# Kernel tuning notes

Measured on AMD Instinct MI355X. Metric: run time of the kernel, lower is better.

The kernel has to match this reference:

```python
import jax, jax.numpy as jnp
import numpy as np

N_HEADS = 32
N_KV_HEADS = 8
HEAD_DIM = 64
ROPE_THETA = 500000.0


def _rope_cos_sin(position_ids, head_dim, theta):
    # position_ids: [pb, S] int -> cos/sin [pb, S, head_dim]
    inv_freq = 1.0 / (theta ** (jnp.arange(0, head_dim, 2, dtype=jnp.float32) / head_dim))
    freqs = position_ids.astype(jnp.float32)[:, :, None] * inv_freq[None, None, :]  # [pb,S,D/2]
    emb = jnp.concatenate([freqs, freqs], axis=-1)  # [pb,S,D]
    return jnp.cos(emb), jnp.sin(emb)


def _rotate_half(x):
    d = x.shape[-1] // 2
    return jnp.concatenate([-x[..., d:], x[..., :d]], axis=-1)


def setup_inputs() -> dict:
    key = jax.random.key(0)
    k1, k2, k3, k4, k5 = jax.random.split(key, 5)
    B, S, H = 1, 2048, 2048
    KVD = N_KV_HEADS * HEAD_DIM
    scale = 0.02
    return {
        "hidden_states": jax.random.normal(k1, (B, S, H), jnp.float32),
        "position_ids": jnp.arange(S, dtype=jnp.int64 if jax.config.jax_enable_x64 else jnp.int32)[None, :],
        "Wq": jax.random.normal(k2, (H, H), jnp.float32) * scale,
        "Wk": jax.random.normal(k3, (H, KVD), jnp.float32) * scale,
        "Wv": jax.random.normal(k4, (H, KVD), jnp.float32) * scale,
        "Wo": jax.random.normal(k5, (H, H), jnp.float32) * scale,
    }


def reference(hidden_states, position_ids, Wq, Wk, Wv, Wo):
    B, S, H = hidden_states.shape
    G = N_HEADS // N_KV_HEADS  # GQA group size

    q = (hidden_states @ Wq).reshape(B, S, N_HEADS, HEAD_DIM).transpose(0, 2, 1, 3)      # [B,Hq,S,D]
    k = (hidden_states @ Wk).reshape(B, S, N_KV_HEADS, HEAD_DIM).transpose(0, 2, 1, 3)   # [B,Hk,S,D]
    v = (hidden_states @ Wv).reshape(B, S, N_KV_HEADS, HEAD_DIM).transpose(0, 2, 1, 3)   # [B,Hk,S,D]

    cos, sin = _rope_cos_sin(position_ids, HEAD_DIM, ROPE_THETA)  # [pb,S,D]
    cos = cos[:, None].astype(hidden_states.dtype)  # [pb,1,S,D] broadcasts over heads
    sin = sin[:, None].astype(hidden_states.dtype)
    q = q * cos + _rotate_half(q) * sin
    k = k * cos + _rotate_half(k) * sin

    # GQA without materializing repeated K/V: group query heads by kv head
    qg = q.reshape(B, N_KV_HEADS, G, S, HEAD_DIM)
    scale = 1.0 / jnp.sqrt(jnp.asarray(HEAD_DIM, hidden_states.dtype))
    scores = jnp.einsum('bkgqd,bksd->bkgqs', qg, k) * scale  # [B,Hk,G,S,S]
    causal = jnp.tril(jnp.ones((S, S), bool))
    scores = jnp.where(causal, scores, jnp.asarray(-jnp.inf, scores.dtype))
    probs = jax.nn.softmax(scores, axis=-1)
    out = jnp.einsum('bkgqs,bksd->bkgqd', probs, v)  # [B,Hk,G,S,D]
    out = out.reshape(B, N_HEADS, S, HEAD_DIM).transpose(0, 2, 1, 3).reshape(B, S, H)
    return out @ Wo
```

## Files before the change

kernel.cpp:

```cpp
#include <hip/hip_runtime.h>
#include <hip/hip_bf16.h>
#include <math.h>

#define S_LEN 2048
#define HID   2048
#define NH    32
#define NKV   8
#define HD    64
#define QKD   2560
#define LOG2E 1.44269504f
#define L2THETA_32 0.591611505f

typedef unsigned short u16;
typedef __attribute__((ext_vector_type(8))) short short8;
typedef __attribute__((ext_vector_type(4))) float f32x4;

__device__ __forceinline__ u16 f2bf(float x) {
    union { __hip_bfloat16 b; u16 u; } c; c.b = __float2bfloat16(x); return c.u;
}
__device__ __forceinline__ float bf2f(u16 u) {
    union { unsigned int i; float f; } c; c.i = ((unsigned int)u) << 16; return c.f;
}
__device__ __forceinline__ void async_copy16(void* lds, const void* g) {
    __builtin_amdgcn_global_load_lds((const __attribute__((address_space(1))) unsigned int*)g,
                                     (__attribute__((address_space(3))) unsigned int*)lds,
                                     16, 0, 0);
}

__global__ __launch_bounds__(256)
void cast_bf16(const float* __restrict__ in, u16* __restrict__ out, int n8) {
    int i = blockIdx.x * blockDim.x + threadIdx.x;
    if (i >= n8) return;
    const float4* p = (const float4*)(in + (size_t)i * 8);
    float4 a = p[0], b = p[1];
    short8 o;
    o[0] = f2bf(a.x); o[1] = f2bf(a.y); o[2] = f2bf(a.z); o[3] = f2bf(a.w);
    o[4] = f2bf(b.x); o[5] = f2bf(b.y); o[6] = f2bf(b.z); o[7] = f2bf(b.w);
    *(short8*)(out + (size_t)i * 8) = o;
}

__global__ __launch_bounds__(256)
void transpose_all(const float* __restrict__ Wq, const float* __restrict__ Wk,
                   const float* __restrict__ Wv, const float* __restrict__ Wo,
                   u16* __restrict__ WqkvT, u16* __restrict__ WoT) {
    const float* W; u16* WT; int Nin, xT;
    switch (blockIdx.z) {
        case 0:  W = Wq; WT = WqkvT;                         Nin = 2048; xT = 64; break;
        case 1:  W = Wk; WT = WqkvT + (size_t)2048 * 2048;   Nin = 512;  xT = 16; break;
        case 2:  W = Wv; WT = WqkvT + (size_t)2560 * 2048;   Nin = 512;  xT = 16; break;
        default: W = Wo; WT = WoT;                           Nin = 2048; xT = 64; break;
    }
    if ((int)blockIdx.x >= xT) return;
    __shared__ float tile[32][33];
    const int tx = threadIdx.x & 31, ty = threadIdx.x >> 5;
    const int x = blockIdx.x * 32 + tx;
#pragma unroll
    for (int j = ty; j < 32; j += 8)
        tile[j][tx] = W[(size_t)(blockIdx.y * 32 + j) * Nin + x];
    __syncthreads();
    const int xo = blockIdx.y * 32 + tx;
#pragma unroll
    for (int j = ty; j < 32; j += 8)
        WT[(size_t)(blockIdx.x * 32 + j) * 2048 + xo] = f2bf(tile[tx][j]);
}

__global__ __launch_bounds__(256)
void rope_qk(u16* __restrict__ QK, const int* __restrict__ pos) {
    int idx = blockIdx.x * blockDim.x + threadIdx.x;
    int d = idx & 31;
    int hh = (idx >> 5) % 40;
    int s = idx / (32 * 40);
    if (s >= S_LEN) return;
    float p = (float)pos[s];
    float inv_freq = exp2f(-(float)d * L2THETA_32);
    float ang = p * inv_freq;
    float c = cosf(ang), sn = sinf(ang);
    float sc = (hh < 32) ? 0.125f * LOG2E : 1.0f;
    u16* b = QK + (size_t)s * QKD + hh * HD;
    float x0 = bf2f(b[d]), x1 = bf2f(b[d + 32]);
    b[d]      = f2bf((x0 * c - x1 * sn) * sc);
    b[d + 32] = f2bf((x1 * c + x0 * sn) * sc);
}

template<int MODE>
__global__ __launch_bounds__(256)
void gemm_bt(const u16* __restrict__ A, const u16* __restrict__ Bt,
             void* __restrict__ Cv, u16* __restrict__ Vt, int M, int N, int K) {
    __shared__ __attribute__((aligned(16))) u16 As[2][8192];
    __shared__ __attribute__((aligned(16))) u16 Bs[2][4096];
    const int t = threadIdx.x;
    const int lane = t & 63;
    const int w = t >> 6;
    const int lm = lane & 15, quad = lane >> 4;
    const int row0 = blockIdx.y * 128, col0 = blockIdx.x * 64;
    const int wr = w * 32;

    f32x4 acc[2][4];
#pragma unroll
    for (int i = 0; i < 2; ++i)
#pragma unroll
        for (int j = 0; j < 4; ++j) acc[i][j] = (f32x4){0.f, 0.f, 0.f, 0.f};

    const size_t strideB = (size_t)K * 2;
    const char* Ab = (const char*)(A + (size_t)row0 * K);
    const char* Bb = (const char*)(Bt + (size_t)col0 * K);

    const int srow = t >> 3;
    const int scswz = ((t & 7) ^ (srow & 7)) * 16;

    auto stage = [&](int ks, int buf) {
        const int k0b = ks * 128;
        char* ad = (char*)As[buf] + t * 16;
        char* bd = (char*)Bs[buf] + t * 16;
#pragma unroll
        for (int i = 0; i < 4; ++i)
            async_copy16(ad + i * 4096, Ab + (size_t)(i * 32 + srow) * strideB + k0b + scswz);
#pragma unroll
        for (int i = 0; i < 2; ++i)
            async_copy16(bd + i * 4096, Bb + (size_t)(i * 32 + srow) * strideB + k0b + scswz);
    };

    const int nk = K >> 6;
    stage(0, 0);
    if (nk > 1) stage(1, 1);

    const int fswz = (quad ^ (lm & 7)) << 4;

    for (int kk = 0; kk < nk; ++kk) {
        const int cur = kk & 1;
        if (kk + 1 < nk) { asm volatile("s_waitcnt vmcnt(6)\ns_barrier" ::: "memory"); }
        else             { asm volatile("s_waitcnt vmcnt(0)\ns_barrier" ::: "memory"); }

        short8 af[2][2], bfv[4][2];
#pragma unroll
        for (int i = 0; i < 2; ++i) {
            const char* ar = (const char*)As[cur] + (wr + 16 * i + lm) * 128;
            af[i][0] = *(const short8*)(ar + fswz);
            af[i][1] = *(const short8*)(ar + (fswz ^ 64));
        }
#pragma unroll
        for (int j = 0; j < 4; ++j) {
            const char* br = (const char*)Bs[cur] + (16 * j + lm) * 128;
            bfv[j][0] = *(const short8*)(br + fswz);
            bfv[j][1] = *(const short8*)(br + (fswz ^ 64));
        }
#pragma unroll
        for (int i = 0; i < 2; ++i)
#pragma unroll
            for (int j = 0; j < 4; ++j) {
                acc[i][j] = __builtin_amdgcn_mfma_f32_16x16x32_bf16(af[i][0], bfv[j][0], acc[i][j], 0, 0, 0);
                acc[i][j] = __builtin_amdgcn_mfma_f32_16x16x32_bf16(af[i][1], bfv[j][1], acc[i][j], 0, 0, 0);
            }

        asm volatile("s_waitcnt lgkmcnt(0)\ns_barrier" ::: "memory");
        if (kk + 2 < nk) stage(kk + 2, cur);
    }

    const int cr = quad * 4;
#pragma unroll
    for (int i = 0; i < 2; ++i) {
        const int gr = row0 + wr + 16 * i + cr;
#pragma unroll
        for (int j = 0; j < 4; ++j) {
            const int gc = col0 + 16 * j + lm;
            if (MODE == 0) {
#pragma unroll
                for (int rr = 0; rr < 4; ++rr)
                    ((float*)Cv)[(size_t)(gr + rr) * N + gc] = acc[i][j][rr];
            } else if (gc < 2560) {
#pragma unroll
                for (int rr = 0; rr < 4; ++rr)
                    ((u16*)Cv)[(size_t)(gr + rr) * QKD + gc] = f2bf(acc[i][j][rr]);
            } else {
                const int d = gc - 2560;
                ushort4 vv;
                vv.x = f2bf(acc[i][j][0]); vv.y = f2bf(acc[i][j][1]);
                vv.z = f2bf(acc[i][j][2]); vv.w = f2bf(acc[i][j][3]);
                *(ushort4*)(Vt + (size_t)d * S_LEN + gr) = vv;
            }
        }
    }
}

__global__ __launch_bounds__(256)
void attn_mfma(const u16* __restrict__ QK, const u16* __restrict__ Vtg,
               u16* __restrict__ Ctx) {
    __shared__ __attribute__((aligned(16))) u16 QPs[4096];
    __shared__ __attribute__((aligned(16))) u16 Ks[2][4096];
    __shared__ __attribute__((aligned(16))) u16 Vts[2][4096];

    const int t = threadIdx.x;
    const int lane = t & 63;
    const int w = t >> 6;
    const int lm = lane & 15, quad = lane >> 4;
    const int qt = (gridDim.x - 1) - blockIdx.x;
    const int h = blockIdx.y;
    const int kh = h >> 2;
    const int q0 = qt * 64;
    const int njt = qt + 1;

    const char* Kb = (const char*)(QK + 2048 + kh * HD);
    const char* Vb = (const char*)(Vtg + (size_t)(kh * 64) * S_LEN);

    const int srow = t >> 3;
    const int scswz = ((t & 7) ^ (srow & 7)) * 16;

    {
        const char* qb = (const char*)(QK + h * HD);
        const int qrow = w * 16 + (lane >> 3);
        const int qcs = ((lane & 7) ^ (lane >> 3)) * 16;
#pragma unroll
        for (int k2 = 0; k2 < 2; ++k2)
            async_copy16((char*)QPs + w * 2048 + k2 * 1024 + lane * 16,
                         qb + (size_t)(q0 + qrow + k2 * 8) * (QKD * 2) + qcs);
    }

    auto stage_kv = [&](int jt_, int buf) {
        const int j0_ = jt_ * 64;
        char* kdst = (char*)Ks + buf * 8192 + t * 16;
        char* vdst = (char*)Vts + buf * 8192 + t * 16;
        async_copy16(kdst,        Kb + (size_t)(j0_ + srow)      * (QKD * 2) + scswz);
        async_copy16(kdst + 4096, Kb + (size_t)(j0_ + 32 + srow) * (QKD * 2) + scswz);
        async_copy16(vdst,        Vb + (size_t)srow        * (S_LEN * 2) + j0_ * 2 + scswz);
        async_copy16(vdst + 4096, Vb + (size_t)(32 + srow) * (S_LEN * 2) + j0_ * 2 + scswz);
    };

    stage_kv(0, 0);
    if (njt > 1) {
        stage_kv(1, 1);
        asm volatile("s_waitcnt vmcnt(8)" ::: "memory");
    } else {
        asm volatile("s_waitcnt vmcnt(4)" ::: "memory");
    }

    const int ra = w * 16 + lm;
    const int fswz = ((quad ^ (lm & 7)) << 4);
    const short8 qa0 = *(const short8*)((const char*)QPs + ra * 128 + fswz);
    const short8 qa1 = *(const short8*)((const char*)QPs + ra * 128 + (fswz ^ 64));
    asm volatile("s_waitcnt lgkmcnt(0)" ::: "memory");

    short8 onesf;
    {
        const short ob = (lm == 0) ? (short)0x3F80 : (short)0;
#pragma unroll
        for (int j = 0; j < 8; ++j) onesf[j] = ob;
    }

    f32x4 oa[4], la;
#pragma unroll
    for (int dt = 0; dt < 4; ++dt) oa[dt] = (f32x4){0.f, 0.f, 0.f, 0.f};
    la = (f32x4){0.f, 0.f, 0.f, 0.f};

    for (int jt = 0; jt < njt; ++jt) {
        const int cur = jt & 1;
        if (jt + 1 < njt) { asm volatile("s_waitcnt vmcnt(4)\ns_barrier" ::: "memory"); }
        else              { asm volatile("s_waitcnt vmcnt(0)\ns_barrier" ::: "memory"); }

        const char* Kc = (const char*)Ks + cur * 8192;
        const char* Vc = (const char*)Vts + cur * 8192;

        f32x4 sa[4];
#pragma unroll
        for (int ct = 0; ct < 4; ++ct)
            sa[ct] = (f32x4){-16.f, -16.f, -16.f, -16.f};
#pragma unroll
        for (int ct = 0; ct < 4; ++ct) {
            const char* kr = Kc + (ct * 16 + lm) * 128;
            short8 kf0 = *(const short8*)(kr + fswz);
            short8 kf1 = *(const short8*)(kr + (fswz ^ 64));
            sa[ct] = __builtin_amdgcn_mfma_f32_16x16x32_bf16(kf0, qa0, sa[ct], 0, 0, 0);
            sa[ct] = __builtin_amdgcn_mfma_f32_16x16x32_bf16(kf1, qa1, sa[ct], 0, 0, 0);
        }
        if (jt == qt) {
#pragma unroll
            for (int ct = 0; ct < 4; ++ct) {
                const int kvl = ct * 16 + quad * 4;
#pragma unroll
                for (int r = 0; r < 4; ++r)
                    if (kvl + r > ra) sa[ct][r] = -1e30f;
            }
        }
#pragma unroll
        for (int ct = 0; ct < 4; ++ct) {
            ushort4 pka;
            pka.x = f2bf(__builtin_amdgcn_exp2f(sa[ct][0]));
            pka.y = f2bf(__builtin_amdgcn_exp2f(sa[ct][1]));
            pka.z = f2bf(__builtin_amdgcn_exp2f(sa[ct][2]));
            pka.w = f2bf(__builtin_amdgcn_exp2f(sa[ct][3]));
            const int pc = (((2 * ct + (quad >> 1)) ^ (lm & 7)) << 4) + ((quad & 1) << 3);
            *(ushort4*)((char*)QPs + ra * 128 + pc) = pka;
        }
        const short8 pa0 = *(const short8*)((const char*)QPs + ra * 128 + fswz);
        const short8 pa1 = *(const short8*)((const char*)QPs + ra * 128 + (fswz ^ 64));
#pragma unroll
        for (int dt = 0; dt < 4; ++dt) {
            const char* vr = Vc + (dt * 16 + lm) * 128;
            short8 vf0 = *(const short8*)(vr + fswz);
            short8 vf1 = *(const short8*)(vr + (fswz ^ 64));
            oa[dt] = __builtin_amdgcn_mfma_f32_16x16x32_bf16(vf0, pa0, oa[dt], 0, 0, 0);
            oa[dt] = __builtin_amdgcn_mfma_f32_16x16x32_bf16(vf1, pa1, oa[dt], 0, 0, 0);
        }
        la = __builtin_amdgcn_mfma_f32_16x16x32_bf16(onesf, pa0, la, 0, 0, 0);
        la = __builtin_amdgcn_mfma_f32_16x16x32_bf16(onesf, pa1, la, 0, 0, 0);

        asm volatile("s_waitcnt lgkmcnt(0)\ns_barrier" ::: "memory");
        if (jt + 2 < njt) stage_kv(jt + 2, cur);
    }

    const float inva = 1.f / __shfl(la[0], lm);
    const int rowa = q0 + ra;
#pragma unroll
    for (int dt = 0; dt < 4; ++dt) {
        ushort4 o;
        o.x = f2bf(oa[dt][0] * inva); o.y = f2bf(oa[dt][1] * inva);
        o.z = f2bf(oa[dt][2] * inva); o.w = f2bf(oa[dt][3] * inva);
        *(ushort4*)(Ctx + (size_t)rowa * HID + h * HD + dt * 16 + quad * 4) = o;
    }
}

extern "C" void kernel_launch(void* const* d_in, const int* in_sizes, int n_in,
                              void* d_out, int out_size, void* d_ws, size_t ws_size,
                              hipStream_t stream) {
    const float* X   = (const float*)d_in[0];
    const int*   pos = (const int*)d_in[1];
    const float* Wq  = (const float*)d_in[2];
    const float* Wk  = (const float*)d_in[3];
    const float* Wv  = (const float*)d_in[4];
    const float* Wo  = (const float*)d_in[5];
    float* out = (float*)d_out;

    u16* Xb    = (u16*)d_ws;
    u16* WqkvT = Xb + (size_t)4194304;
    u16* WoT   = WqkvT + (size_t)6291456;
    u16* QK    = WoT + (size_t)4194304;
    u16* Vt    = QK + (size_t)S_LEN * QKD;
    u16* Ctxb  = Xb;

    cast_bf16<<<2048, 256, 0, stream>>>(X, Xb, 524288);
    transpose_all<<<dim3(64, 64, 4), 256, 0, stream>>>(Wq, Wk, Wv, Wo, WqkvT, WoT);

    gemm_bt<1><<<dim3(48, 16), 256, 0, stream>>>(Xb, WqkvT, QK, Vt, 2048, 3072, 2048);

    rope_qk<<<10240, 256, 0, stream>>>(QK, pos);

    attn_mfma<<<dim3(32, 32), 256, 0, stream>>>(QK, Vt, Ctxb);

    gemm_bt<0><<<dim3(32, 16), 256, 0, stream>>>(Ctxb, WoT, out, nullptr, 2048, 2048, 2048);
}
```

Baseline: 230.2 us.

## Fuse RoPE into QKV GEMM epilogue and merge cast with weight transpose

Applies the rotary embedding and the softmax scale directly in the QKV GEMM epilogue, using the fact that each 64-column block holds one whole head. This removes the separate rope kernel and its read-modify-write pass over QK. The activation cast is also folded into the weight-transpose launch as an extra z-slice, saving one launch. The cost is more transcendental math in the GEMM epilogue, and the result is now rounded to bf16 once instead of twice.

```diff
diff --git a/kernel.cpp b/kernel.cpp
--- a/kernel.cpp
+++ b/kernel.cpp
@@ -28,21 +28,21 @@
 }
 
 __global__ __launch_bounds__(256)
-void cast_bf16(const float* __restrict__ in, u16* __restrict__ out, int n8) {
-    int i = blockIdx.x * blockDim.x + threadIdx.x;
-    if (i >= n8) return;
-    const float4* p = (const float4*)(in + (size_t)i * 8);
-    float4 a = p[0], b = p[1];
-    short8 o;
-    o[0] = f2bf(a.x); o[1] = f2bf(a.y); o[2] = f2bf(a.z); o[3] = f2bf(a.w);
-    o[4] = f2bf(b.x); o[5] = f2bf(b.y); o[6] = f2bf(b.z); o[7] = f2bf(b.w);
-    *(short8*)(out + (size_t)i * 8) = o;
-}
-
-__global__ __launch_bounds__(256)
-void transpose_all(const float* __restrict__ Wq, const float* __restrict__ Wk,
-                   const float* __restrict__ Wv, const float* __restrict__ Wo,
-                   u16* __restrict__ WqkvT, u16* __restrict__ WoT) {
+void prep(const float* __restrict__ X, u16* __restrict__ Xb,
+          const float* __restrict__ Wq, const float* __restrict__ Wk,
+          const float* __restrict__ Wv, const float* __restrict__ Wo,
+          u16* __restrict__ WqkvT, u16* __restrict__ WoT) {
+    if (blockIdx.z == 4) {
+        const int i = (blockIdx.y * 64 + (int)blockIdx.x) * 256 + threadIdx.x;
+        if (i >= 524288) return;
+        const float4* p = (const float4*)(X + (size_t)i * 8);
+        float4 a = p[0], b = p[1];
+        short8 o;
+        o[0] = f2bf(a.x); o[1] = f2bf(a.y); o[2] = f2bf(a.z); o[3] = f2bf(a.w);
+        o[4] = f2bf(b.x); o[5] = f2bf(b.y); o[6] = f2bf(b.z); o[7] = f2bf(b.w);
+        *(short8*)(Xb + (size_t)i * 8) = o;
+        return;
+    }
     const float* W; u16* WT; int Nin, xT;
     switch (blockIdx.z) {
         case 0:  W = Wq; WT = WqkvT;                         Nin = 2048; xT = 64; break;
@@ -64,28 +64,11 @@
         WT[(size_t)(blockIdx.x * 32 + j) * 2048 + xo] = f2bf(tile[tx][j]);
 }
 
-__global__ __launch_bounds__(256)
-void rope_qk(u16* __restrict__ QK, const int* __restrict__ pos) {
-    int idx = blockIdx.x * blockDim.x + threadIdx.x;
-    int d = idx & 31;
-    int hh = (idx >> 5) % 40;
-    int s = idx / (32 * 40);
-    if (s >= S_LEN) return;
-    float p = (float)pos[s];
-    float inv_freq = exp2f(-(float)d * L2THETA_32);
-    float ang = p * inv_freq;
-    float c = cosf(ang), sn = sinf(ang);
-    float sc = (hh < 32) ? 0.125f * LOG2E : 1.0f;
-    u16* b = QK + (size_t)s * QKD + hh * HD;
-    float x0 = bf2f(b[d]), x1 = bf2f(b[d + 32]);
-    b[d]      = f2bf((x0 * c - x1 * sn) * sc);
-    b[d + 32] = f2bf((x1 * c + x0 * sn) * sc);
-}
-
 template<int MODE>
 __global__ __launch_bounds__(256)
 void gemm_bt(const u16* __restrict__ A, const u16* __restrict__ Bt,
-             void* __restrict__ Cv, u16* __restrict__ Vt, int M, int N, int K) {
+             void* __restrict__ Cv, u16* __restrict__ Vt,
+             const int* __restrict__ pos, int M, int N, int K) {
     __shared__ __attribute__((aligned(16))) u16 As[2][8192];
     __shared__ __attribute__((aligned(16))) u16 Bs[2][4096];
     const int t = threadIdx.x;
@@ -157,26 +140,51 @@
     }
 
     const int cr = quad * 4;
-#pragma unroll
-    for (int i = 0; i < 2; ++i) {
-        const int gr = row0 + wr + 16 * i + cr;
-#pragma unroll
-        for (int j = 0; j < 4; ++j) {
-            const int gc = col0 + 16 * j + lm;
-            if (MODE == 0) {
+    if (MODE == 0) {
+#pragma unroll
+        for (int i = 0; i < 2; ++i) {
+            const int gr = row0 + wr + 16 * i + cr;
+#pragma unroll
+            for (int j = 0; j < 4; ++j) {
+                const int gc = col0 + 16 * j + lm;
 #pragma unroll
                 for (int rr = 0; rr < 4; ++rr)
                     ((float*)Cv)[(size_t)(gr + rr) * N + gc] = acc[i][j][rr];
-            } else if (gc < 2560) {
-#pragma unroll
-                for (int rr = 0; rr < 4; ++rr)
-                    ((u16*)Cv)[(size_t)(gr + rr) * QKD + gc] = f2bf(acc[i][j][rr]);
-            } else {
-                const int d = gc - 2560;
+            }
+        }
+    } else if (col0 >= 2560) {
+#pragma unroll
+        for (int i = 0; i < 2; ++i) {
+            const int gr = row0 + wr + 16 * i + cr;
+#pragma unroll
+            for (int j = 0; j < 4; ++j) {
+                const int d = col0 + 16 * j + lm - 2560;
                 ushort4 vv;
                 vv.x = f2bf(acc[i][j][0]); vv.y = f2bf(acc[i][j][1]);
                 vv.z = f2bf(acc[i][j][2]); vv.w = f2bf(acc[i][j][3]);
                 *(ushort4*)(Vt + (size_t)d * S_LEN + gr) = vv;
+            }
+        }
+    } else {
+        const float qsc = (col0 < 2048) ? 0.125f * LOG2E : 1.0f;
+        const float invf0 = exp2f(-(float)lm * L2THETA_32);
+        const float invf1 = exp2f(-(float)(16 + lm) * L2THETA_32);
+#pragma unroll
+        for (int i = 0; i < 2; ++i) {
+            const int gr = row0 + wr + 16 * i + cr;
+#pragma unroll
+            for (int rr = 0; rr < 4; ++rr) {
+                const float p = (float)pos[gr + rr];
+                const float a0 = p * invf0, a1 = p * invf1;
+                const float c0 = cosf(a0), s0 = sinf(a0);
+                const float c1 = cosf(a1), s1 = sinf(a1);
+                const float x00 = acc[i][0][rr], x02 = acc[i][2][rr];
+                const float x01 = acc[i][1][rr], x03 = acc[i][3][rr];
+                u16* outr = (u16*)Cv + (size_t)(gr + rr) * QKD + col0 + lm;
+                outr[0]  = f2bf((x00 * c0 - x02 * s0) * qsc);
+                outr[32] = f2bf((x02 * c0 + x00 * s0) * qsc);
+                outr[16] = f2bf((x01 * c1 - x03 * s1) * qsc);
+                outr[48] = f2bf((x03 * c1 + x01 * s1) * qsc);
             }
         }
     }
@@ -336,14 +344,11 @@
     u16* Vt    = QK + (size_t)S_LEN * QKD;
     u16* Ctxb  = Xb;
 
-    cast_bf16<<<2048, 256, 0, stream>>>(X, Xb, 524288);
-    transpose_all<<<dim3(64, 64, 4), 256, 0, stream>>>(Wq, Wk, Wv, Wo, WqkvT, WoT);
-
-    gemm_bt<1><<<dim3(48, 16), 256, 0, stream>>>(Xb, WqkvT, QK, Vt, 2048, 3072, 2048);
-
-    rope_qk<<<10240, 256, 0, stream>>>(QK, pos);
+    prep<<<dim3(64, 64, 5), 256, 0, stream>>>(X, Xb, Wq, Wk, Wv, Wo, WqkvT, WoT);
+
+    gemm_bt<1><<<dim3(48, 16), 256, 0, stream>>>(Xb, WqkvT, QK, Vt, pos, 2048, 3072, 2048);
 
     attn_mfma<<<dim3(32, 32), 256, 0, stream>>>(QK, Vt, Ctxb);
 
-    gemm_bt<0><<<dim3(32, 16), 256, 0, stream>>>(Ctxb, WoT, out, nullptr, 2048, 2048, 2048);
-}
+    gemm_bt<0><<<dim3(32, 16), 256, 0, stream>>>(Ctxb, WoT, out, nullptr, pos, 2048, 2048, 2048);
+}
```

Measured after the change: 218.9 us. 4.9% less time.
